# Kernel tuning notes

Measured on AMD Instinct MI355X. Metric: run time of the kernel, lower is better.

## Reference

```python
import jax, jax.numpy as jnp
import numpy as np

TEMP = 0.07
LN_EPS = 1e-5


def _l2norm(x, eps=1e-12):
    n = jnp.linalg.norm(x, axis=-1, keepdims=True)
    return x / jnp.maximum(n, eps)


def setup_inputs() -> dict:
    key = jax.random.key(0)
    ks = jax.random.split(key, 8)
    B, N, D, S = 1024, 100000, 1024, 2
    scale = 1.0 / np.sqrt(D)
    return {
        "q": jax.random.normal(ks[0], (B, D), jnp.float32),
        "bank_values": jax.random.normal(ks[1], (N, D), jnp.float32),
        "proj_w": jax.random.normal(ks[2], (S, D, D), jnp.float32) * scale,
        "proj_b": jax.random.normal(ks[3], (S, D), jnp.float32) * 0.01,
        "unify_w": jax.random.normal(ks[4], (S, D, D), jnp.float32) * scale,
        "unify_b": jax.random.normal(ks[5], (S, D), jnp.float32) * 0.01,
        "ln_gamma": jnp.ones((D,), jnp.float32),
        "ln_beta": jnp.zeros((D,), jnp.float32),
        "top_m": 32,
    }


def reference(q, bank_values, proj_w, proj_b, unify_w, unify_b, ln_gamma, ln_beta, top_m):
    # PrototypeBank.build: keys = L2-normalized values (detached)
    keys = _l2norm(bank_values)  # [N, D]
    num_scales = proj_w.shape[0]
    ref = jnp.zeros_like(q)
    for s in range(num_scales):  # small fixed structural loop
        p = q @ proj_w[s].T + proj_b[s]                       # [B, D] Linear
        scores = _l2norm(p) @ keys.T                          # [B, N] cosine
        top_s, top_i = jax.lax.top_k(scores, top_m)           # [B, m]
        attn = jax.nn.softmax(top_s / TEMP, axis=-1)          # [B, m]
        z = jnp.einsum('bm,bmd->bd', attn, bank_values[top_i])  # weighted gather-sum
        ref = ref + z @ unify_w[s].T + unify_b[s]
    mu = ref.mean(axis=-1, keepdims=True)
    var = ref.var(axis=-1, keepdims=True)
    out = (ref - mu) * jax.lax.rsqrt(var + LN_EPS) * ln_gamma + ln_beta
    return out
```

## Files before the change

kernel.cpp:

```cpp
#include <hip/hip_runtime.h>
#include <math.h>


static inline size_t align256(size_t x){ return (x + 255) & ~size_t(255); }

typedef short bf16x8 __attribute__((ext_vector_type(8)));
typedef float f32x4  __attribute__((ext_vector_type(4)));

#define GLOAD_LDS16(gp, lp) \
  __builtin_amdgcn_global_load_lds((const __attribute__((address_space(1))) unsigned int*)(gp), \
                                   (__attribute__((address_space(3))) unsigned int*)(lp), 16, 0, 0)

__device__ inline unsigned short f2bf(float f){
  unsigned int u = __float_as_uint(f);
  u += 0x7fffu + ((u >> 16) & 1u);
  return (unsigned short)(u >> 16);
}
__device__ inline float bf2f(unsigned int h16){
  return __uint_as_float(h16 << 16);
}

template<bool SCALE_OUT>
__global__ __launch_bounds__(256) void rnorm_convert_kernel(
    const float* __restrict__ X, float* __restrict__ rn,
    unsigned short* __restrict__ out, int rows, int D)
{
  int wv = threadIdx.x >> 6, lane = threadIdx.x & 63;
  int r = blockIdx.x * 4 + wv;
  if (r >= rows) return;
  const float4* xr = (const float4*)(X + (size_t)r * D);
  int nv = D >> 2;
  float ss = 0.f;
  for (int i = lane; i < nv; i += 64){
    float4 v = xr[i];
    ss = fmaf(v.x,v.x, fmaf(v.y,v.y, fmaf(v.z,v.z, fmaf(v.w,v.w, ss))));
  }
  #pragma unroll
  for (int off = 32; off; off >>= 1) ss += __shfl_xor(ss, off);
  float rinv = 1.f / fmaxf(sqrtf(ss), 1e-12f);
  if (lane == 0) rn[r] = rinv;
  const float sc = SCALE_OUT ? rinv : 1.f;
  unsigned short* orow = out + (size_t)r * D;
  for (int i = lane; i < (D >> 3); i += 64){
    float4 v0 = xr[i*2], v1 = xr[i*2+1];
    v0.x*=sc; v0.y*=sc; v0.z*=sc; v0.w*=sc;
    v1.x*=sc; v1.y*=sc; v1.z*=sc; v1.w*=sc;
    uint4 w;
    w.x = (unsigned)f2bf(v0.x) | ((unsigned)f2bf(v0.y) << 16);
    w.y = (unsigned)f2bf(v0.z) | ((unsigned)f2bf(v0.w) << 16);
    w.z = (unsigned)f2bf(v1.x) | ((unsigned)f2bf(v1.y) << 16);
    w.w = (unsigned)f2bf(v1.z) | ((unsigned)f2bf(v1.w) << 16);
    *(uint4*)(orow + i*8) = w;
  }
}

template<int RM, int RN, bool ACCUM>
__global__ __launch_bounds__(256) void gemm_nt_kernel(
    const float* __restrict__ A, const float* __restrict__ B,
    const float* __restrict__ bias, const float* __restrict__ bscale,
    float* __restrict__ C, int M, int Nn, int K, int Brows, int ldc)
{
  __shared__ float As[16][RM*64 + 4];
  __shared__ float Bs[16][RN*64 + 4];
  const int t  = threadIdx.x;
  const int tm = t >> 4, tn = t & 15;
  const int m0 = blockIdx.y * (RM*64), n0 = blockIdx.x * (RN*64);

  float acc[RM][RN][4][4];
  #pragma unroll
  for (int r=0;r<RM;++r)
    #pragma unroll
    for (int c=0;c<RN;++c)
      #pragma unroll
      for (int i=0;i<4;++i)
        #pragma unroll
        for (int j=0;j<4;++j) acc[r][c][i][j]=0.f;

  for (int kp = 0; kp < K; kp += 16){
    #pragma unroll
    for (int l = 0; l < RM; ++l){
      int li = t + l*256;
      int row = li >> 2, kq = (li & 3) << 2;
      float4 v = *(const float4*)(A + (size_t)(m0+row)*K + kp + kq);
      As[kq+0][row]=v.x; As[kq+1][row]=v.y; As[kq+2][row]=v.z; As[kq+3][row]=v.w;
    }
    #pragma unroll
    for (int l = 0; l < RN; ++l){
      int li = t + l*256;
      int row = li >> 2, kq = (li & 3) << 2;
      int gn = n0 + row;
      float4 v = make_float4(0.f,0.f,0.f,0.f);
      float sc = 1.f;
      if (gn < Brows){
        v = *(const float4*)(B + (size_t)gn*K + kp + kq);
        if (bscale) sc = bscale[gn];
      }
      Bs[kq+0][row]=v.x*sc; Bs[kq+1][row]=v.y*sc; Bs[kq+2][row]=v.z*sc; Bs[kq+3][row]=v.w*sc;
    }
    __syncthreads();
    #pragma unroll
    for (int kk = 0; kk < 16; ++kk){
      float av[RM][4], bv[RN][4];
      #pragma unroll
      for (int r=0;r<RM;++r){
        float4 a = *(const float4*)&As[kk][r*64 + tm*4];
        av[r][0]=a.x; av[r][1]=a.y; av[r][2]=a.z; av[r][3]=a.w;
      }
      #pragma unroll
      for (int c=0;c<RN;++c){
        float4 b = *(const float4*)&Bs[kk][c*64 + tn*4];
        bv[c][0]=b.x; bv[c][1]=b.y; bv[c][2]=b.z; bv[c][3]=b.w;
      }
      #pragma unroll
      for (int r=0;r<RM;++r)
        #pragma unroll
        for (int c=0;c<RN;++c)
          #pragma unroll
          for (int i=0;i<4;++i)
            #pragma unroll
            for (int j=0;j<4;++j)
              acc[r][c][i][j] = fmaf(av[r][i], bv[c][j], acc[r][c][i][j]);
    }
    __syncthreads();
  }

  #pragma unroll
  for (int r=0;r<RM;++r){
    #pragma unroll
    for (int i=0;i<4;++i){
      int gm = m0 + r*64 + tm*4 + i;
      #pragma unroll
      for (int c=0;c<RN;++c){
        int gn = n0 + c*64 + tn*4;
        if (gn >= Nn) continue;
        float* cp = C + (size_t)gm*ldc + gn;
        float o0=acc[r][c][i][0], o1=acc[r][c][i][1], o2=acc[r][c][i][2], o3=acc[r][c][i][3];
        if (gn + 3 < Nn){
          float4 o = make_float4(o0,o1,o2,o3);
          if (bias){ float4 bb = *(const float4*)&bias[gn]; o.x+=bb.x; o.y+=bb.y; o.z+=bb.z; o.w+=bb.w; }
          if (ACCUM){ float4 cc = *(const float4*)cp; o.x+=cc.x; o.y+=cc.y; o.z+=cc.z; o.w+=cc.w; }
          *(float4*)cp = o;
        } else {
          float ov[4] = {o0,o1,o2,o3};
          for (int j=0;j<4;++j){
            if (gn + j < Nn){
              float o = ov[j];
              if (bias)  o += bias[gn+j];
              if (ACCUM) o += cp[j];
              cp[j] = o;
            }
          }
        }
      }
    }
  }
}

__global__ __launch_bounds__(256) void scores_mfma_kernel(
    const unsigned short* __restrict__ Abf, const unsigned short* __restrict__ Bbf,
    unsigned short* __restrict__ C, int M, int Nn, int K, int ldc)
{
  __shared__ __align__(16) unsigned char smem[32768];

  const int t = threadIdx.x;
  const int lane = t & 63, wid = t >> 6;
  const int wm = wid >> 1, wn = wid & 1;
  const int l15 = lane & 15, l4 = lane >> 4;
  const int m0 = blockIdx.x * 128, n0 = blockIdx.y * 128;

  f32x4 acc[4][4];
  #pragma unroll
  for (int i=0;i<4;++i)
    #pragma unroll
    for (int j=0;j<4;++j) acc[i][j] = (f32x4)0.f;

  const int srow = t >> 3;
  const int sb   = (t & 7) * 16;
  const int ldsb = wid * 1024;

  for (int kp = 0; kp < K; kp += 64){
    #pragma unroll
    for (int i = 0; i < 4; ++i){
      int row = srow + i*32;
      int src = sb ^ ((row & 7) << 4);
      const unsigned char* ga = (const unsigned char*)Abf
          + ((size_t)(m0+row)*K + kp)*2 + src;
      GLOAD_LDS16(ga, smem + i*4096 + ldsb);
      int gn = n0 + row; if (gn >= Nn) gn = Nn - 1;
      const unsigned char* gb = (const unsigned char*)Bbf
          + ((size_t)gn*K + kp)*2 + src;
      GLOAD_LDS16(gb, smem + 16384 + i*4096 + ldsb);
    }
    __syncthreads();

    const unsigned char* As_ = smem;
    const unsigned char* Bs_ = smem + 16384;
    bf16x8 B0[4], B1[4];
    #pragma unroll
    for (int fn = 0; fn < 4; ++fn){
      int br = wn*64 + fn*16 + l15;
      int xr = (br & 7) << 4;
      const unsigned char* bp = Bs_ + br*128;
      B0[fn] = *(const bf16x8*)(bp + (( l4*16      ) ^ xr));
      B1[fn] = *(const bf16x8*)(bp + ((64 + l4*16 ) ^ xr));
    }
    #pragma unroll
    for (int fm = 0; fm < 4; ++fm){
      int ar = wm*64 + fm*16 + l15;
      int xr = (ar & 7) << 4;
      const unsigned char* ap = As_ + ar*128;
      bf16x8 A0 = *(const bf16x8*)(ap + (( l4*16      ) ^ xr));
      bf16x8 A1 = *(const bf16x8*)(ap + ((64 + l4*16 ) ^ xr));
      #pragma unroll
      for (int fn = 0; fn < 4; ++fn){
        acc[fm][fn] = __builtin_amdgcn_mfma_f32_16x16x32_bf16(A0, B0[fn], acc[fm][fn], 0,0,0);
        acc[fm][fn] = __builtin_amdgcn_mfma_f32_16x16x32_bf16(A1, B1[fn], acc[fm][fn], 0,0,0);
      }
    }
    __syncthreads();
  }

  unsigned char* ep = smem + wid*8192;
  #pragma unroll
  for (int fm = 0; fm < 4; ++fm){
    #pragma unroll
    for (int fn = 0; fn < 4; ++fn){
      #pragma unroll
      for (int r = 0; r < 4; ++r){
        int row  = fm*16 + l4*4 + r;
        int colb = (fn*16 + l15) * 2;
        *(unsigned short*)(ep + row*128 + (colb ^ ((row & 7) << 4))) = f2bf(acc[fm][fn][r]);
      }
    }
  }
  __syncthreads();
  const int gr0 = m0 + wm*64, gc0 = n0 + wn*64;
  #pragma unroll
  for (int it = 0; it < 8; ++it){
    int slot = it*64 + lane;
    int row  = slot >> 3;
    int q    = (slot & 7) * 16;
    uint4 v = *(const uint4*)(ep + row*128 + q);
    int lq = q ^ ((row & 7) << 4);
    int gcol = gc0 + (lq >> 1);
    int grow = gr0 + row;
    if (gcol + 7 < Nn){
      *(uint4*)(C + (size_t)grow*ldc + gcol) = v;
    } else {
      unsigned short tmp[8];
      *(uint4*)tmp = v;
      for (int j = 0; j < 8; ++j)
        if (gcol + j < Nn) C[(size_t)grow*ldc + gcol + j] = tmp[j];
    }
  }
}

__global__ __launch_bounds__(256) void chunk_filter_kernel(
    const unsigned short* __restrict__ scores, int ldc, int colbase, int Nwindow,
    int NC, float* __restrict__ cand_s, int* __restrict__ cand_i,
    int chunk0, int nchunks_total, int cap, float eps)
{
  extern __shared__ float lds[];
  __shared__ float sv[256];
  __shared__ float tau_s;
  __shared__ int cnt;
  const int row = blockIdx.x, t = threadIdx.x;
  const int lc = blockIdx.y;
  const int col0l = lc * NC;
  int ncols = Nwindow - col0l; if (ncols > NC) ncols = NC;
  const int gchunk = chunk0 + lc;
  const unsigned short* sr = scores + (size_t)row * ldc + col0l;

  float m0 = -INFINITY, m1 = -INFINITY, m2 = -INFINITY, m3 = -INFINITY;
  const int nc8 = ncols >> 3;
  const uint4* sr8 = (const uint4*)sr;
  float4* lds4 = (float4*)lds;
  for (int j = t; j < nc8; j += 256){
    uint4 v = sr8[j];
    float4 a = make_float4(bf2f(v.x & 0xffffu), bf2f(v.x >> 16),
                           bf2f(v.y & 0xffffu), bf2f(v.y >> 16));
    float4 b = make_float4(bf2f(v.z & 0xffffu), bf2f(v.z >> 16),
                           bf2f(v.w & 0xffffu), bf2f(v.w >> 16));
    lds4[j*2]   = a;
    lds4[j*2+1] = b;
    m0 = fmaxf(m0, fmaxf(a.x, b.x)); m1 = fmaxf(m1, fmaxf(a.y, b.y));
    m2 = fmaxf(m2, fmaxf(a.z, b.z)); m3 = fmaxf(m3, fmaxf(a.w, b.w));
  }
  for (int j = (nc8 << 3) + t; j < ncols; j += 256){
    float v = bf2f((unsigned)sr[j]);
    lds[j] = v;
    m0 = fmaxf(m0, v);
  }
  sv[t] = fmaxf(fmaxf(m0, m1), fmaxf(m2, m3));
  __syncthreads();

  for (int k = 2; k <= 256; k <<= 1){
    for (int j = k >> 1; j > 0; j >>= 1){
      int p = t ^ j;
      float a = sv[t], b = sv[p];
      bool up = ((t & k) == 0);
      float keep = (t < p) ? (up ? fmaxf(a,b) : fminf(a,b))
                           : (up ? fminf(a,b) : fmaxf(a,b));
      __syncthreads();
      sv[t] = keep;
      __syncthreads();
    }
  }
  if (t == 0){ tau_s = sv[31]; cnt = 0; }
  __syncthreads();
  const float thr = tau_s - eps;

  float* cs = cand_s + ((size_t)row * nchunks_total + gchunk) * cap;
  int*   ci = cand_i + ((size_t)row * nchunks_total + gchunk) * cap;

  for (int j = t; j < ncols; j += 256){
    float v = lds[j];
    if (v >= thr){
      int pos = atomicAdd(&cnt, 1);
      if (pos < cap){ cs[pos] = v; ci[pos] = colbase + col0l + j; }
    }
  }
  __syncthreads();
  int n = cnt < cap ? cnt : cap;
  for (int j = n + t; j < cap; j += 256) ci[j] = -1;
}

__global__ __launch_bounds__(256) void select_softmax_gather_kernel(
    const float* __restrict__ cand_s, const int* __restrict__ cand_i,
    const float* __restrict__ p, const float* __restrict__ rn_bank,
    const float* __restrict__ pnorm, const float* __restrict__ bank,
    float* __restrict__ z, int ncap, int D, int topm, float invtemp, float eps)
{
  __shared__ float p_s[1024];
  __shared__ float vs[1024]; __shared__ int vi[1024];
  __shared__ float sv[256];
  __shared__ int   cidx[256];
  __shared__ float rv[256];
  __shared__ float tau_s;
  __shared__ int cnt;
  const int row = blockIdx.x, t = threadIdx.x;
  const int lane = t & 63, wid = t >> 6;

  const float4* pr = (const float4*)(p + (size_t)row * D);
  for (int i = t; i < (D >> 2); i += 256) ((float4*)p_s)[i] = pr[i];
  const float* cs = cand_s + (size_t)row * ncap;
  const int*  ci = cand_i + (size_t)row * ncap;
  for (int j = t; j < ncap; j += 256){
    int k = ci[j];
    vi[j] = k;
    vs[j] = (k >= 0) ? cs[j] : -INFINITY;
  }
  __syncthreads();

  float m = -INFINITY;
  for (int j = t; j < ncap; j += 256) m = fmaxf(m, vs[j]);
  sv[t] = m;
  __syncthreads();
  for (int k = 2; k <= 256; k <<= 1){
    for (int j = k >> 1; j > 0; j >>= 1){
      int pp = t ^ j;
      float a = sv[t], b = sv[pp];
      bool up = ((t & k) == 0);
      float keep = (t < pp) ? (up ? fmaxf(a,b) : fminf(a,b))
                            : (up ? fminf(a,b) : fmaxf(a,b));
      __syncthreads();
      sv[t] = keep;
      __syncthreads();
    }
  }
  if (t == 0){ tau_s = sv[31]; cnt = 0; }
  __syncthreads();
  const float thr = tau_s - eps;

  for (int j = t; j < ncap; j += 256){
    if (vi[j] >= 0 && vs[j] >= thr){
      int pos = atomicAdd(&cnt, 1);
      if (pos < 256) cidx[pos] = vi[j];
    }
  }
  __syncthreads();
  const int n2 = cnt < 256 ? cnt : 256;
  rv[t] = -INFINITY;
  if (t >= n2) cidx[t] = 0x7fffffff;
  __syncthreads();

  const int nj = D >> 8;
  for (int c = wid; c < n2; c += 4){
    int idx = cidx[c];
    const float4* kr = (const float4*)(bank + (size_t)idx * D);
    float ss = 0.f;
    for (int j = 0; j < nj; ++j){
      float4 kv = kr[lane + j*64];
      float4 pv = *(const float4*)&p_s[(lane + j*64) << 2];
      ss = fmaf(pv.x,kv.x, fmaf(pv.y,kv.y, fmaf(pv.z,kv.z, fmaf(pv.w,kv.w, ss))));
    }
    #pragma unroll
    for (int off = 32; off; off >>= 1) ss += __shfl_xor(ss, off);
    if (lane == 0) rv[c] = ss * rn_bank[idx];
  }
  __syncthreads();

  for (int k = 2; k <= 256; k <<= 1){
    for (int j = k >> 1; j > 0; j >>= 1){
      int pp = t ^ j;
      float av = rv[t];  int ai = cidx[t];
      float bv = rv[pp]; int bi = cidx[pp];
      bool up = ((t & k) == 0);
      bool agtb = (av > bv) || (av == bv && ai < bi);
      bool keepA = (t < pp) ? (up ? agtb : !agtb)
                            : (up ? !agtb : agtb);
      __syncthreads();
      if (keepA){ rv[t] = av; cidx[t] = ai; } else { rv[t] = bv; cidx[t] = bi; }
      __syncthreads();
    }
  }

  if (t == 0){
    float pn = pnorm[row] * invtemp;
    float mx = rv[0] * pn;
    float sum = 0.f;
    for (int i = 0; i < topm; ++i){
      float w = expf(rv[i]*pn - mx);
      sv[i] = w; sum += w;
    }
    float inv = 1.f / sum;
    for (int i = 0; i < topm; ++i) sv[i] *= inv;
  }
  __syncthreads();

  for (int d4 = t; d4 < (D >> 2); d4 += 256){
    float ax=0.f, ay=0.f, az=0.f, aw=0.f;
    for (int i = 0; i < topm; ++i){
      float a = sv[i];
      const float4 v = *(const float4*)(bank + (size_t)cidx[i]*D + (d4<<2));
      ax = fmaf(a, v.x, ax); ay = fmaf(a, v.y, ay);
      az = fmaf(a, v.z, az); aw = fmaf(a, v.w, aw);
    }
    *(float4*)(z + (size_t)row*D + (d4<<2)) = make_float4(ax,ay,az,aw);
  }
}

__global__ __launch_bounds__(256) void layernorm_kernel(
    const float* __restrict__ ref, const float* __restrict__ gamma,
    const float* __restrict__ beta, float* __restrict__ out, int D, float eps)
{
  __shared__ float s1[4], s2[4];
  const int row = blockIdx.x, t = threadIdx.x;
  const float4* xr = (const float4*)(ref + (size_t)row*D);
  int nv = D >> 2;
  float sum = 0.f, ssq = 0.f;
  for (int i = t; i < nv; i += 256){
    float4 v = xr[i];
    sum += v.x+v.y+v.z+v.w;
    ssq = fmaf(v.x,v.x, fmaf(v.y,v.y, fmaf(v.z,v.z, fmaf(v.w,v.w, ssq))));
  }
  const int lane = t & 63, wid = t >> 6;
  #pragma unroll
  for (int off = 32; off; off >>= 1){ sum += __shfl_xor(sum, off); ssq += __shfl_xor(ssq, off); }
  if (lane == 0){ s1[wid] = sum; s2[wid] = ssq; }
  __syncthreads();
  sum = s1[0]+s1[1]+s1[2]+s1[3];
  ssq = s2[0]+s2[1]+s2[2]+s2[3];
  float mu  = sum / (float)D;
  float var = ssq / (float)D - mu*mu;
  float rs  = rsqrtf(var + eps);
  const float4* g4 = (const float4*)gamma;
  const float4* b4 = (const float4*)beta;
  float4* o4 = (float4*)(out + (size_t)row*D);
  for (int i = t; i < nv; i += 256){
    float4 v = xr[i], g = g4[i], bb = b4[i];
    float4 o;
    o.x = (v.x-mu)*rs*g.x + bb.x;
    o.y = (v.y-mu)*rs*g.y + bb.y;
    o.z = (v.z-mu)*rs*g.z + bb.z;
    o.w = (v.w-mu)*rs*g.w + bb.w;
    o4[i] = o;
  }
}

extern "C" void kernel_launch(void* const* d_in, const int* in_sizes, int n_in,
                              void* d_out, int out_size, void* d_ws, size_t ws_size,
                              hipStream_t stream)
{
  const float* q       = (const float*)d_in[0];
  const float* bank    = (const float*)d_in[1];
  const float* proj_w  = (const float*)d_in[2];
  const float* proj_b  = (const float*)d_in[3];
  const float* unify_w = (const float*)d_in[4];
  const float* unify_b = (const float*)d_in[5];
  const float* gamma   = (const float*)d_in[6];
  const float* beta    = (const float*)d_in[7];

  const int D = in_sizes[6];
  const int B = in_sizes[0] / D;
  const int N = in_sizes[1] / D;
  const int S = in_sizes[2] / (D * D);
  const int R = S * B;
  const int TOPM = 32;
  const int CAP  = 64;
  const int NC   = 12544;
  const float INVTEMP = 1.0f / 0.07f;
  const float EPS = 0.025f;

  const int NCH = (N + NC - 1) / NC;

  char* wsb = (char*)d_ws;
  size_t off = 0;
  auto take = [&](size_t bytes)->char*{ char* p = wsb + off; off += align256(bytes); return p; };
  float* rn_bank = (float*)take((size_t)N*4);
  float* pnorm   = (float*)take((size_t)R*4);
  float* p       = (float*)take((size_t)R*D*4);
  float* z       = (float*)take((size_t)R*D*4);
  float* ref     = (float*)take((size_t)B*D*4);
  float* cand_s  = (float*)take((size_t)R*NCH*CAP*4);
  int*   cand_i  = (int*)  take((size_t)R*NCH*CAP*4);
  unsigned short* bank_bf = (unsigned short*)take((size_t)N*D*2);
  unsigned short* p_bf    = (unsigned short*)take((size_t)R*D*2);
  unsigned short* scores  = (unsigned short*)take((size_t)R*(size_t)N*2);

  rnorm_convert_kernel<true><<<(N+3)/4, 256, 0, stream>>>(
      bank, rn_bank, bank_bf, N, D);

  dim3 g1(D/64, B/64);
  for (int s = 0; s < S; ++s)
    gemm_nt_kernel<1,1,false><<<g1, 256, 0, stream>>>(
        q, proj_w + (size_t)s*D*D, proj_b + (size_t)s*D, nullptr,
        p + (size_t)s*B*D, B, D, D, D, D);

  rnorm_convert_kernel<false><<<(R+3)/4, 256, 0, stream>>>(
      p, pnorm, p_bf, R, D);

  {
    dim3 g2(R/128, (N + 127)/128);
    scores_mfma_kernel<<<g2, 256, 0, stream>>>(
        p_bf, bank_bf, scores, R, N, D, N);
    chunk_filter_kernel<<<dim3(R, NCH), 256, (size_t)NC*4, stream>>>(
        scores, N, 0, N, NC, cand_s, cand_i,
        0, NCH, CAP, EPS);
  }

  select_softmax_gather_kernel<<<R, 256, 0, stream>>>(
      cand_s, cand_i, p, rn_bank, pnorm, bank, z,
      NCH*CAP, D, TOPM, INVTEMP, EPS);

  for (int s = 0; s < S; ++s){
    if (s == 0)
      gemm_nt_kernel<1,1,false><<<g1, 256, 0, stream>>>(
          z + (size_t)s*B*D, unify_w + (size_t)s*D*D, unify_b + (size_t)s*D, nullptr,
          ref, B, D, D, D, D);
    else
      gemm_nt_kernel<1,1,true><<<g1, 256, 0, stream>>>(
          z + (size_t)s*B*D, unify_w + (size_t)s*D*D, unify_b + (size_t)s*D, nullptr,
          ref, B, D, D, D, D);
  }

  layernorm_kernel<<<B, 256, 0, stream>>>(ref, gamma, beta, (float*)d_out, D, 1e-5f);
}
```

Before: 1.396 ms.

## Remap score GEMM blocks per XCD and store outputs directly from registers

```diff
diff --git a/kernel.cpp b/kernel.cpp
--- a/kernel.cpp
+++ b/kernel.cpp
@@ -166,7 +166,14 @@
   const int lane = t & 63, wid = t >> 6;
   const int wm = wid >> 1, wn = wid & 1;
   const int l15 = lane & 15, l4 = lane >> 4;
-  const int m0 = blockIdx.x * 128, n0 = blockIdx.y * 128;
+
+  const int nwg = gridDim.x;
+  const int q = nwg >> 3, r = nwg & 7;
+  const int xcd = blockIdx.x & 7, idx = blockIdx.x >> 3;
+  const int logical = (xcd < r ? xcd*(q+1) : r*(q+1) + (xcd-r)*q) + idx;
+  const int mtiles = M >> 7;
+  const int m0 = (logical % mtiles) * 128;
+  const int n0 = (logical / mtiles) * 128;
 
   f32x4 acc[4][4];
   #pragma unroll
@@ -220,37 +227,17 @@
     __syncthreads();
   }
 
-  unsigned char* ep = smem + wid*8192;
   #pragma unroll
   for (int fm = 0; fm < 4; ++fm){
+    int row = m0 + wm*64 + fm*16 + l4*4;
     #pragma unroll
     for (int fn = 0; fn < 4; ++fn){
-      #pragma unroll
-      for (int r = 0; r < 4; ++r){
-        int row  = fm*16 + l4*4 + r;
-        int colb = (fn*16 + l15) * 2;
-        *(unsigned short*)(ep + row*128 + (colb ^ ((row & 7) << 4))) = f2bf(acc[fm][fn][r]);
+      int col = n0 + wn*64 + fn*16 + l15;
+      if (col < Nn){
+        unsigned short* cp = C + (size_t)row*ldc + col;
+        #pragma unroll
+        for (int r2 = 0; r2 < 4; ++r2) cp[(size_t)r2*ldc] = f2bf(acc[fm][fn][r2]);
       }
-    }
-  }
-  __syncthreads();
-  const int gr0 = m0 + wm*64, gc0 = n0 + wn*64;
-  #pragma unroll
-  for (int it = 0; it < 8; ++it){
-    int slot = it*64 + lane;
-    int row  = slot >> 3;
-    int q    = (slot & 7) * 16;
-    uint4 v = *(const uint4*)(ep + row*128 + q);
-    int lq = q ^ ((row & 7) << 4);
-    int gcol = gc0 + (lq >> 1);
-    int grow = gr0 + row;
-    if (gcol + 7 < Nn){
-      *(uint4*)(C + (size_t)grow*ldc + gcol) = v;
-    } else {
-      unsigned short tmp[8];
-      *(uint4*)tmp = v;
-      for (int j = 0; j < 8; ++j)
-        if (gcol + j < Nn) C[(size_t)grow*ldc + gcol + j] = tmp[j];
     }
   }
 }
@@ -531,8 +518,9 @@
       p, pnorm, p_bf, R, D);
 
   {
-    dim3 g2(R/128, (N + 127)/128);
-    scores_mfma_kernel<<<g2, 256, 0, stream>>>(
+    int ntile = (N + 127) / 128;
+    int nwg = (R / 128) * ntile;
+    scores_mfma_kernel<<<nwg, 256, 0, stream>>>(
         p_bf, bank_bf, scores, R, N, D, N);
     chunk_filter_kernel<<<dim3(R, NCH), 256, (size_t)NC*4, stream>>>(
         scores, N, 0, N, NC, cand_s, cand_i,
```

Result: no change. 1.398 ms (+0.1%).
